# Kernel tuning notes

Hardware: AMD Instinct MI355X
Metric: run time of the kernel (lower is better)

## Reference

```python
import jax, jax.numpy as jnp
import numpy as np

NUM_HEADS = 8
NUM_GROUPS = 32
EPS = 1e-4


def group_norm(x, scale, bias):
    # x: [b, L, C]; normalize over (L, channels-within-group) per flax GroupNorm
    b, l, c = x.shape
    xg = x.reshape(b, l, NUM_GROUPS, c // NUM_GROUPS)
    mean = jnp.mean(xg, axis=(1, 3), keepdims=True)
    var = jnp.var(xg, axis=(1, 3), keepdims=True)
    xg = (xg - mean) * jax.lax.rsqrt(var + EPS)
    return xg.reshape(b, l, c) * scale + bias


def setup_inputs() -> dict:
    key = jax.random.key(0)
    ks = jax.random.split(key, 6)
    bs, L, C = 4, 1024, 512
    hf = C // NUM_HEADS  # 64
    x = jax.random.normal(ks[0], (bs, L, C), dtype=jnp.float32)
    W_qkv = jax.random.normal(ks[1], (C, C * 2), dtype=jnp.float32) * (1.0 / C)
    gn_qkv_scale = jnp.ones((C * 2,), dtype=jnp.float32)
    gn_qkv_bias = jnp.zeros((C * 2,), dtype=jnp.float32)
    rel_emb = jax.random.normal(ks[2], (hf * 2, 2 * L - 1), dtype=jnp.float32) * (1.0 / hf)
    gn_out_scale = jnp.ones((C,), dtype=jnp.float32)
    gn_out_bias = jnp.zeros((C,), dtype=jnp.float32)
    return {
        "x": x,
        "W_qkv": W_qkv,
        "gn_qkv_scale": gn_qkv_scale,
        "gn_qkv_bias": gn_qkv_bias,
        "rel_emb": rel_emb,
        "gn_out_scale": gn_out_scale,
        "gn_out_bias": gn_out_bias,
    }


def reference(x, W_qkv, gn_qkv_scale, gn_qkv_bias, rel_emb, gn_out_scale, gn_out_bias):
    bs, L, C = x.shape
    hf = C // NUM_HEADS
    qkv = x @ W_qkv                                # [b, L, 2C]
    qkv = group_norm(qkv, gn_qkv_scale, gn_qkv_bias)
    qkv = qkv.reshape(bs, L, NUM_HEADS, hf * 2).transpose((0, 2, 3, 1))  # [b,h,2hf,L]
    q = qkv[:, :, : hf // 2]          # [b,h,hf/2,L]
    k = qkv[:, :, hf // 2: hf]        # [b,h,hf/2,L]
    v = qkv[:, :, hf:]                # [b,h,hf,L]
    # relative distance index: rel[i,j] = i - j + L - 1
    rel_idx = jnp.arange(L)[:, None] - jnp.arange(L)[None, :] + (L - 1)
    rpe = rel_emb[:, rel_idx]         # [2hf, L, L]
    rpe_q = rpe[: hf // 2]
    rpe_k = rpe[hf // 2: hf]
    rpe_v = rpe[hf:]
    logits = (
        jnp.einsum('bhdi,bhdj->bhij', q, k)
        + jnp.einsum('bhdi,dij->bhij', q, rpe_k)
        + jnp.einsum('bhdi,dij->bhij', k, rpe_q)
    )
    attn = jax.nn.softmax(logits, axis=3).astype(jnp.float32)
    wv = jnp.einsum('bhij,bhdj->bhdi', attn, v)
    wve = jnp.einsum('bhij,dij->bhdi', attn, rpe_v)
    out = (wv + wve).transpose((0, 3, 1, 2)).reshape(bs, L, C)
    return group_norm(out, gn_out_scale, gn_out_bias)
```

## Files before the change

### kernel.cpp

```cpp
#include <hip/hip_runtime.h>
#include <hip/hip_bf16.h>

typedef unsigned short ushort;
typedef __attribute__((ext_vector_type(8))) short bf16x8;
typedef __attribute__((ext_vector_type(4))) float f32x4;
typedef __attribute__((ext_vector_type(4))) unsigned short ushort4v;

#define BSZ  4
#define LSEQ 1024
#define CIN  512
#define C2   1024
#define NH   8
#define GEPS 1e-4f

static __device__ __forceinline__ ushort f2b(float f) {
    __hip_bfloat16 h = __float2bfloat16(f);
    return *reinterpret_cast<ushort*>(&h);
}
static __device__ __forceinline__ float b2f(ushort u) {
    __hip_bfloat16 h = *reinterpret_cast<__hip_bfloat16*>(&u);
    return __bfloat162float(h);
}

__global__ __launch_bounds__(256) void prep_xsplit(const float* __restrict__ x,
                                                   ushort* __restrict__ xh,
                                                   ushort* __restrict__ xl) {
    const size_t i4 = (size_t)blockIdx.x * 256 + threadIdx.x;
    const float4 v = *reinterpret_cast<const float4*>(&x[i4 * 4]);
    ushort4v h, lo;
    const float vv[4] = {v.x, v.y, v.z, v.w};
    #pragma unroll
    for (int c = 0; c < 4; ++c) {
        const ushort hh = f2b(vv[c]);
        h[c] = hh;
        lo[c] = f2b(vv[c] - b2f(hh));
    }
    *reinterpret_cast<ushort4v*>(&xh[i4 * 4]) = h;
    *reinterpret_cast<ushort4v*>(&xl[i4 * 4]) = lo;
}

__global__ __launch_bounds__(256) void prep_wT(const float* __restrict__ W,
                                               ushort* __restrict__ wth,
                                               ushort* __restrict__ wtl) {
    __shared__ float tl[64][65];
    const int k0 = blockIdx.y * 64, n0 = blockIdx.x * 64;
    const int t = threadIdx.x;
    #pragma unroll
    for (int u = 0; u < 16; ++u) {
        const int idx = t + 256 * u;
        const int kk = idx >> 6, nn = idx & 63;
        tl[kk][nn] = W[(size_t)(k0 + kk) * 1024 + n0 + nn];
    }
    __syncthreads();
    #pragma unroll
    for (int u = 0; u < 16; ++u) {
        const int idx = t + 256 * u;
        const int nn = idx >> 6, kk = idx & 63;
        const float v = tl[kk][nn];
        const ushort h = f2b(v);
        wth[(size_t)(n0 + nn) * 512 + k0 + kk] = h;
        wtl[(size_t)(n0 + nn) * 512 + k0 + kk] = f2b(v - b2f(h));
    }
}

__global__ __launch_bounds__(256) void prep_rel(const float* __restrict__ rel,
                                                ushort* __restrict__ relT,
                                                ushort* __restrict__ relV) {
    const int t = threadIdx.x;
    if (blockIdx.x < 32) {
        __shared__ float tl[64][65];
        const int r0 = blockIdx.x * 64;
        #pragma unroll
        for (int u = 0; u < 16; ++u) {
            const int idx = t + 256 * u;
            const int dd = idx >> 6, rr = idx & 63;
            int r = r0 + rr; if (r > 2046) r = 2046;
            tl[dd][rr] = rel[(size_t)(dd ^ 32) * 2047 + r];
        }
        __syncthreads();
        #pragma unroll
        for (int u = 0; u < 16; ++u) {
            const int idx = t + 256 * u;
            const int rr = idx >> 6, dd = idx & 63;
            relT[(size_t)(r0 + rr) * 64 + dd] = f2b(tl[dd][rr]);
        }
    } else {
        const int idx = (blockIdx.x - 32) * 256 + t;
        const int dv = idx >> 11, r = idx & 2047;
        const int rc = r > 2046 ? 2046 : r;
        relV[(size_t)dv * 2048 + r] = f2b(rel[(size_t)(64 + dv) * 2047 + rc]);
    }
}

__global__ __launch_bounds__(256) void gemm_qkv_mfma(const ushort* __restrict__ xh,
                                                     const ushort* __restrict__ xl,
                                                     const ushort* __restrict__ wth,
                                                     const ushort* __restrict__ wtl,
                                                     float* __restrict__ qkv,
                                                     float* __restrict__ sumq) {
    __shared__ ushort Ah[128][40];
    __shared__ ushort Al[128][40];
    __shared__ ushort Bh[128][40];
    __shared__ ushort Bl[128][40];
    const int t = threadIdx.x;
    const int w = t >> 6, l = t & 63;
    const int lr = l & 15, lq = l >> 4;
    const int wm = w >> 1, wn = w & 1;
    const int m0 = blockIdx.y * 128, n0 = blockIdx.x * 128;
    const int b = m0 >> 10;
    f32x4 acc[4][4] = {};
    for (int k0 = 0; k0 < 512; k0 += 32) {
        __syncthreads();
        #pragma unroll
        for (int u = 0; u < 2; ++u) {
            const int idx = t + 256 * u;
            const int r = idx >> 2, c16 = (idx & 3) * 8;
            *(bf16x8*)&Ah[r][c16] = *(const bf16x8*)&xh[(size_t)(m0 + r) * 512 + k0 + c16];
            *(bf16x8*)&Al[r][c16] = *(const bf16x8*)&xl[(size_t)(m0 + r) * 512 + k0 + c16];
            *(bf16x8*)&Bh[r][c16] = *(const bf16x8*)&wth[(size_t)(n0 + r) * 512 + k0 + c16];
            *(bf16x8*)&Bl[r][c16] = *(const bf16x8*)&wtl[(size_t)(n0 + r) * 512 + k0 + c16];
        }
        __syncthreads();
        bf16x8 ah[4], av[4];
        #pragma unroll
        for (int mi = 0; mi < 4; ++mi) {
            ah[mi] = *(const bf16x8*)&Ah[64 * wm + 16 * mi + lr][8 * lq];
            av[mi] = *(const bf16x8*)&Al[64 * wm + 16 * mi + lr][8 * lq];
        }
        #pragma unroll
        for (int ni = 0; ni < 4; ++ni) {
            const bf16x8 bh = *(const bf16x8*)&Bh[64 * wn + 16 * ni + lr][8 * lq];
            const bf16x8 bl = *(const bf16x8*)&Bl[64 * wn + 16 * ni + lr][8 * lq];
            #pragma unroll
            for (int mi = 0; mi < 4; ++mi) {
                f32x4 a = acc[mi][ni];
                a = __builtin_amdgcn_mfma_f32_16x16x32_bf16(ah[mi], bl, a, 0, 0, 0);
                a = __builtin_amdgcn_mfma_f32_16x16x32_bf16(av[mi], bh, a, 0, 0, 0);
                a = __builtin_amdgcn_mfma_f32_16x16x32_bf16(ah[mi], bh, a, 0, 0, 0);
                acc[mi][ni] = a;
            }
        }
    }
    #pragma unroll
    for (int mi = 0; mi < 4; ++mi)
        #pragma unroll
        for (int ni = 0; ni < 4; ++ni)
            #pragma unroll
            for (int e = 0; e < 4; ++e)
                qkv[(size_t)(m0 + 64 * wm + 16 * mi + 4 * lq + e) * 1024 + n0 + 64 * wn + 16 * ni + lr] = acc[mi][ni][e];
    #pragma unroll
    for (int ni = 0; ni < 4; ++ni) {
        float s = 0.f, s2 = 0.f;
        #pragma unroll
        for (int mi = 0; mi < 4; ++mi)
            #pragma unroll
            for (int e = 0; e < 4; ++e) { const float v = acc[mi][ni][e]; s += v; s2 += v * v; }
        #pragma unroll
        for (int o = 32; o; o >>= 1) { s += __shfl_xor(s, o, 64); s2 += __shfl_xor(s2, o, 64); }
        if (l == 0) {
            const int g = (n0 + 64 * wn + 16 * ni) >> 5;
            atomicAdd(&sumq[(b * 32 + g) * 2 + 0], s);
            atomicAdd(&sumq[(b * 32 + g) * 2 + 1], s2);
        }
    }
}

__global__ __launch_bounds__(256) void gn_apply_bf(const float* __restrict__ qkv,
                                                   const float* __restrict__ sumq,
                                                   const float* __restrict__ scale,
                                                   const float* __restrict__ bias,
                                                   ushort* __restrict__ qg,
                                                   ushort* __restrict__ qlo,
                                                   ushort* __restrict__ vb) {
    __shared__ float tile[64][65];
    const int b  = blockIdx.z;
    const int l0 = blockIdx.y * 64, c0 = blockIdx.x * 64;
    const int t  = threadIdx.x;
    const bool vhalf = (c0 & 64);
    const int h = c0 >> 7;
    #pragma unroll
    for (int u = 0; u < 16; ++u) {
        const int idx = t + 256 * u;
        const int lr = idx >> 6, cr = idx & 63;
        const int c = c0 + cr, g = c >> 5;
        const float s  = sumq[(b * 32 + g) * 2 + 0];
        const float s2 = sumq[(b * 32 + g) * 2 + 1];
        const float mu = s * (1.f / 32768.f);
        const float rr = rsqrtf(fmaxf(s2 * (1.f / 32768.f) - mu * mu, 0.f) + GEPS);
        float v = qkv[(size_t)(b * LSEQ + l0 + lr) * C2 + c];
        v = (v - mu) * rr * scale[c] + bias[c];
        const ushort hi = f2b(v);
        qg[(size_t)(b * LSEQ + l0 + lr) * C2 + c] = hi;
        if (vhalf) tile[lr][cr] = v;
        else qlo[(size_t)(b * LSEQ + l0 + lr) * 512 + h * 64 + cr] = f2b(v - b2f(hi));
    }
    if (vhalf) {
        __syncthreads();
        #pragma unroll
        for (int u = 0; u < 16; ++u) {
            const int idx = t + 256 * u;
            const int cw = idx >> 6, lw = idx & 63;
            vb[((size_t)((b * NH + h) * 64 + cw)) * LSEQ + l0 + lw] = f2b(tile[lw][cw]);
        }
    }
}

__global__ __launch_bounds__(256) void attn_mfma(const ushort* __restrict__ qg,
                                                 const ushort* __restrict__ qlo,
                                                 const ushort* __restrict__ vbuf,
                                                 const ushort* __restrict__ relT,
                                                 const ushort* __restrict__ relV,
                                                 float* __restrict__ aout,
                                                 float* __restrict__ sumo) {
    __shared__ __align__(16) ushort rT[128][72];
    __shared__ __align__(16) ushort rV[64][136];
    __shared__ __align__(16) ushort vj[64][72];
    __shared__ __align__(16) ushort TUb[4][16][88];
    __shared__ __align__(16) ushort Ps[4][16][72];
    __shared__ __align__(16) ushort Pr[4][16][104];

    const int t = threadIdx.x;
    const int w = t >> 6, l = t & 63;
    const int lr = l & 15, lq = l >> 4;
    const int i0 = blockIdx.x * 64;
    const int h = blockIdx.y, b = blockIdx.z;
    const int ck0 = w >> 1;

    const size_t arow = (size_t)(b * LSEQ + i0 + 16 * w + lr);
    const bf16x8 a_q  = *(const bf16x8*)&qg[arow * C2 + h * 128 + 8 * lq];
    const bf16x8 a_k  = *(const bf16x8*)&qg[arow * C2 + h * 128 + 32 + 8 * lq];
    const bf16x8 a_ql = *(const bf16x8*)&qlo[arow * 512 + h * 64 + 8 * lq];

    {
        uint* pz = (uint*)&Pr[w][0][0];
        #pragma unroll
        for (int u = 0; u < 13; ++u) pz[l + 64 * u] = 0;
    }

    float m_r[4], l_r[4];
    #pragma unroll
    for (int e = 0; e < 4; ++e) { m_r[e] = -3.0e38f; l_r[e] = 0.f; }
    f32x4 Oa[4] = {};

    const size_t vbase = (size_t)((b * NH + h) * 64) * LSEQ;
    const int tbase = 4 * lq + 63 - lr;
    const int prbase = 16 * w - 32 * ck0 + 63 + 4 * lq - lr;

    for (int j0 = 0; j0 < LSEQ; j0 += 64) {
        const int r0 = i0 - j0 + 960;
        __syncthreads();
        #pragma unroll
        for (int u = 0; u < 4; ++u) {
            const int idx = t + 256 * u;
            const int rl = idx >> 3, c8 = (idx & 7) * 8;
            *(bf16x8*)&rT[rl][c8] = *(const bf16x8*)&relT[(size_t)(r0 + rl) * 64 + c8];
        }
        #pragma unroll
        for (int u = 0; u < 4; ++u) {
            const int idx = t + 256 * u;
            const int dv = idx >> 4, c8 = (idx & 15) * 8;
            *(bf16x8*)&rV[dv][c8] = *(const bf16x8*)&relV[(size_t)dv * 2048 + r0 + c8];
        }
        #pragma unroll
        for (int u = 0; u < 2; ++u) {
            const int idx = t + 256 * u;
            const int dv = idx >> 3, c8 = (idx & 7) * 8;
            *(bf16x8*)&vj[dv][c8] = *(const bf16x8*)&vbuf[vbase + (size_t)dv * LSEQ + j0 + c8];
        }
        __syncthreads();

        #pragma unroll
        for (int ct5 = 0; ct5 < 5; ++ct5) {
            const int rr = 16 * (w + ct5) + lr;
            f32x4 acc = {0.f, 0.f, 0.f, 0.f};
            acc = __builtin_amdgcn_mfma_f32_16x16x32_bf16(a_q, *(const bf16x8*)&rT[rr][8 * lq], acc, 0, 0, 0);
            acc = __builtin_amdgcn_mfma_f32_16x16x32_bf16(a_k, *(const bf16x8*)&rT[rr][32 + 8 * lq], acc, 0, 0, 0);
            #pragma unroll
            for (int e = 0; e < 4; ++e) TUb[w][4 * lq + e][16 * ct5 + lr] = f2b(acc[e]);
        }

        f32x4 sv[4];
        #pragma unroll
        for (int n = 0; n < 4; ++n) {
            const size_t krow = (size_t)(b * LSEQ + j0 + 16 * n + lr);
            const bf16x8 b_hi = *(const bf16x8*)&qg[krow * C2 + h * 128 + 32 + 8 * lq];
            const bf16x8 b_lo = *(const bf16x8*)&qlo[krow * 512 + h * 64 + 32 + 8 * lq];
            f32x4 acc = {0.f, 0.f, 0.f, 0.f};
            acc = __builtin_amdgcn_mfma_f32_16x16x32_bf16(a_q,  b_lo, acc, 0, 0, 0);
            acc = __builtin_amdgcn_mfma_f32_16x16x32_bf16(a_ql, b_hi, acc, 0, 0, 0);
            acc = __builtin_amdgcn_mfma_f32_16x16x32_bf16(a_q,  b_hi, acc, 0, 0, 0);
            #pragma unroll
            for (int e = 0; e < 4; ++e) acc[e] += b2f(TUb[w][4 * lq + e][tbase + e - 16 * n]);
            sv[n] = acc;
        }

        float mx[4];
        #pragma unroll
        for (int e = 0; e < 4; ++e)
            mx[e] = fmaxf(fmaxf(sv[0][e], sv[1][e]), fmaxf(sv[2][e], sv[3][e]));
        #pragma unroll
        for (int o = 1; o < 16; o <<= 1)
            #pragma unroll
            for (int e = 0; e < 4; ++e) mx[e] = fmaxf(mx[e], __shfl_xor(mx[e], o, 64));
        float alpha[4], ssum[4];
        #pragma unroll
        for (int e = 0; e < 4; ++e) {
            const float mn = fmaxf(m_r[e], mx[e]);
            alpha[e] = __expf(m_r[e] - mn);
            m_r[e] = mn;
            ssum[e] = 0.f;
        }
        #pragma unroll
        for (int n = 0; n < 4; ++n)
            #pragma unroll
            for (int e = 0; e < 4; ++e) {
                const float p = __expf(sv[n][e] - m_r[e]);
                ssum[e] += p;
                const ushort pb = f2b(p);
                Ps[w][4 * lq + e][16 * n + lr] = pb;
                Pr[w][4 * lq + e][prbase + e - 16 * n] = pb;
            }
        #pragma unroll
        for (int o = 1; o < 16; o <<= 1)
            #pragma unroll
            for (int e = 0; e < 4; ++e) ssum[e] += __shfl_xor(ssum[e], o, 64);
        #pragma unroll
        for (int e = 0; e < 4; ++e) l_r[e] = l_r[e] * alpha[e] + ssum[e];

        const bf16x8 pa0 = *(const bf16x8*)&Ps[w][lr][8 * lq];
        const bf16x8 pa1 = *(const bf16x8*)&Ps[w][lr][32 + 8 * lq];
        bf16x8 pra[3];
        #pragma unroll
        for (int kk = 0; kk < 3; ++kk) pra[kk] = *(const bf16x8*)&Pr[w][lr][32 * kk + 8 * lq];
        #pragma unroll
        for (int n = 0; n < 4; ++n) {
            f32x4 acc = Oa[n];
            #pragma unroll
            for (int e = 0; e < 4; ++e) acc[e] *= alpha[e];
            acc = __builtin_amdgcn_mfma_f32_16x16x32_bf16(pa0, *(const bf16x8*)&vj[16 * n + lr][8 * lq], acc, 0, 0, 0);
            acc = __builtin_amdgcn_mfma_f32_16x16x32_bf16(pa1, *(const bf16x8*)&vj[16 * n + lr][32 + 8 * lq], acc, 0, 0, 0);
            #pragma unroll
            for (int kk = 0; kk < 3; ++kk) {
                const bf16x8 brv = *(const bf16x8*)&rV[16 * n + lr][32 * (ck0 + kk) + 8 * lq];
                acc = __builtin_amdgcn_mfma_f32_16x16x32_bf16(pra[kk], brv, acc, 0, 0, 0);
            }
            Oa[n] = acc;
        }
    }

    #pragma unroll
    for (int n = 0; n < 4; ++n) {
        float s = 0.f, s2 = 0.f;
        #pragma unroll
        for (int e = 0; e < 4; ++e) {
            const float o = Oa[n][e] / l_r[e];
            aout[((size_t)(b * LSEQ + i0 + 16 * w + 4 * lq + e)) * CIN + h * 64 + 16 * n + lr] = o;
            s += o; s2 += o * o;
        }
        #pragma unroll
        for (int o = 32; o; o >>= 1) { s += __shfl_xor(s, o, 64); s2 += __shfl_xor(s2, o, 64); }
        if (l == 0) {
            atomicAdd(&sumo[(b * 32 + h * 4 + n) * 2 + 0], s);
            atomicAdd(&sumo[(b * 32 + h * 4 + n) * 2 + 1], s2);
        }
    }
}

__global__ __launch_bounds__(256) void gn_out_apply(const float* __restrict__ aout,
                                                    const float* __restrict__ sumo,
                                                    const float* __restrict__ scale,
                                                    const float* __restrict__ bias,
                                                    float* __restrict__ out) {
    const int idx4 = blockIdx.x * 256 + threadIdx.x;
    const int c = (idx4 & 127) * 4;
    const size_t row = idx4 >> 7;
    const int b = (int)(row >> 10);
    const int g = c >> 4;
    const float s  = sumo[(b * 32 + g) * 2 + 0];
    const float s2 = sumo[(b * 32 + g) * 2 + 1];
    const float mu = s * (1.f / 16384.f);
    const float rr = rsqrtf(fmaxf(s2 * (1.f / 16384.f) - mu * mu, 0.f) + GEPS);
    const float4 v = *reinterpret_cast<const float4*>(&aout[row * 512 + c]);
    const float4 sc = *reinterpret_cast<const float4*>(&scale[c]);
    const float4 bi = *reinterpret_cast<const float4*>(&bias[c]);
    float4 o;
    o.x = (v.x - mu) * rr * sc.x + bi.x;
    o.y = (v.y - mu) * rr * sc.y + bi.y;
    o.z = (v.z - mu) * rr * sc.z + bi.z;
    o.w = (v.w - mu) * rr * sc.w + bi.w;
    *reinterpret_cast<float4*>(&out[row * 512 + c]) = o;
}

extern "C" void kernel_launch(void* const* d_in, const int* in_sizes, int n_in,
                              void* d_out, int out_size, void* d_ws, size_t ws_size,
                              hipStream_t stream) {
    (void)in_sizes; (void)n_in; (void)out_size; (void)ws_size;
    const float* x   = (const float*)d_in[0];
    const float* W   = (const float*)d_in[1];
    const float* gqs = (const float*)d_in[2];
    const float* gqb = (const float*)d_in[3];
    const float* rel = (const float*)d_in[4];
    const float* gos = (const float*)d_in[5];
    const float* gob = (const float*)d_in[6];
    float* out = (float*)d_out;

    char* ws = (char*)d_ws;
    float*  qkv  = (float*)ws;
    ushort* qg   = (ushort*)(ws + (16u << 20));
    ushort* vb   = (ushort*)(ws + (24u << 20));
    ushort* rTb  = (ushort*)(ws + (28u << 20));
    ushort* rVb  = (ushort*)(ws + (28u << 20) + (256u << 10));
    ushort* qlo  = (ushort*)(ws + (28u << 20) + (512u << 10));
    float*  aout = (float*)ws;
    float*  stats = (float*)(ws + (32u << 20) + (512u << 10));
    float* sumq = stats;
    float* sumo = stats + 256;
    ushort* xhi = (ushort*)(ws + (16u << 20));
    ushort* xlo = (ushort*)(ws + (20u << 20));
    ushort* wth = (ushort*)(ws + (24u << 20));
    ushort* wtl = (ushort*)(ws + (25u << 20));

    hipMemsetAsync(stats, 0, 2048, stream);
    prep_xsplit<<<2048, 256, 0, stream>>>(x, xhi, xlo);
    prep_wT<<<dim3(16, 8), 256, 0, stream>>>(W, wth, wtl);
    prep_rel<<<544, 256, 0, stream>>>(rel, rTb, rVb);
    gemm_qkv_mfma<<<dim3(8, 32), 256, 0, stream>>>(xhi, xlo, wth, wtl, qkv, sumq);
    gn_apply_bf<<<dim3(16, 16, BSZ), 256, 0, stream>>>(qkv, sumq, gqs, gqb, qg, qlo, vb);
    attn_mfma<<<dim3(16, NH, BSZ), 256, 0, stream>>>(qg, qlo, vb, rTb, rVb, aout, sumo);
    gn_out_apply<<<2048, 256, 0, stream>>>(aout, sumo, gos, gob, out);
}
```

Measured before the change: 231.9 us.

## Split attention over key halves per block, read operands from global, halve GEMM N tile

The attention kernel now gives each pair of waves one 16-row query tile and splits the key range between them. Each wave runs its own online softmax and the two partial results are merged through shared memory at the end. The shared-memory staging of rel embeddings and V is removed: MFMA operands are loaded straight from global/L2, and per-wave scratch is merged into one buffer to cut LDS use and allow more blocks per CU. The QKV GEMM tile shrinks from 128x128 to 128x64 so the grid doubles. This trades more redundant global loads and an extra merge step for more parallelism and occupancy.

```diff
diff --git a/kernel.cpp b/kernel.cpp
--- a/kernel.cpp
+++ b/kernel.cpp
@@ -100,15 +100,14 @@
                                                      float* __restrict__ sumq) {
     __shared__ ushort Ah[128][40];
     __shared__ ushort Al[128][40];
-    __shared__ ushort Bh[128][40];
-    __shared__ ushort Bl[128][40];
+    __shared__ ushort Bh[64][40];
+    __shared__ ushort Bl[64][40];
     const int t = threadIdx.x;
     const int w = t >> 6, l = t & 63;
     const int lr = l & 15, lq = l >> 4;
-    const int wm = w >> 1, wn = w & 1;
-    const int m0 = blockIdx.y * 128, n0 = blockIdx.x * 128;
+    const int m0 = blockIdx.y * 128, n0 = blockIdx.x * 64;
     const int b = m0 >> 10;
-    f32x4 acc[4][4] = {};
+    f32x4 acc[2][4] = {};
     for (int k0 = 0; k0 < 512; k0 += 32) {
         __syncthreads();
         #pragma unroll
@@ -117,22 +116,25 @@
             const int r = idx >> 2, c16 = (idx & 3) * 8;
             *(bf16x8*)&Ah[r][c16] = *(const bf16x8*)&xh[(size_t)(m0 + r) * 512 + k0 + c16];
             *(bf16x8*)&Al[r][c16] = *(const bf16x8*)&xl[(size_t)(m0 + r) * 512 + k0 + c16];
+        }
+        {
+            const int r = t >> 2, c16 = (t & 3) * 8;
             *(bf16x8*)&Bh[r][c16] = *(const bf16x8*)&wth[(size_t)(n0 + r) * 512 + k0 + c16];
             *(bf16x8*)&Bl[r][c16] = *(const bf16x8*)&wtl[(size_t)(n0 + r) * 512 + k0 + c16];
         }
         __syncthreads();
-        bf16x8 ah[4], av[4];
-        #pragma unroll
-        for (int mi = 0; mi < 4; ++mi) {
-            ah[mi] = *(const bf16x8*)&Ah[64 * wm + 16 * mi + lr][8 * lq];
-            av[mi] = *(const bf16x8*)&Al[64 * wm + 16 * mi + lr][8 * lq];
+        bf16x8 ah[2], av[2];
+        #pragma unroll
+        for (int mi = 0; mi < 2; ++mi) {
+            ah[mi] = *(const bf16x8*)&Ah[32 * w + 16 * mi + lr][8 * lq];
+            av[mi] = *(const bf16x8*)&Al[32 * w + 16 * mi + lr][8 * lq];
         }
         #pragma unroll
         for (int ni = 0; ni < 4; ++ni) {
-            const bf16x8 bh = *(const bf16x8*)&Bh[64 * wn + 16 * ni + lr][8 * lq];
-            const bf16x8 bl = *(const bf16x8*)&Bl[64 * wn + 16 * ni + lr][8 * lq];
-            #pragma unroll
-            for (int mi = 0; mi < 4; ++mi) {
+            const bf16x8 bh = *(const bf16x8*)&Bh[16 * ni + lr][8 * lq];
+            const bf16x8 bl = *(const bf16x8*)&Bl[16 * ni + lr][8 * lq];
+            #pragma unroll
+            for (int mi = 0; mi < 2; ++mi) {
                 f32x4 a = acc[mi][ni];
                 a = __builtin_amdgcn_mfma_f32_16x16x32_bf16(ah[mi], bl, a, 0, 0, 0);
                 a = __builtin_amdgcn_mfma_f32_16x16x32_bf16(av[mi], bh, a, 0, 0, 0);
@@ -142,23 +144,23 @@
         }
     }
     #pragma unroll
-    for (int mi = 0; mi < 4; ++mi)
+    for (int mi = 0; mi < 2; ++mi)
         #pragma unroll
         for (int ni = 0; ni < 4; ++ni)
             #pragma unroll
             for (int e = 0; e < 4; ++e)
-                qkv[(size_t)(m0 + 64 * wm + 16 * mi + 4 * lq + e) * 1024 + n0 + 64 * wn + 16 * ni + lr] = acc[mi][ni][e];
+                qkv[(size_t)(m0 + 32 * w + 16 * mi + 4 * lq + e) * 1024 + n0 + 16 * ni + lr] = acc[mi][ni][e];
     #pragma unroll
     for (int ni = 0; ni < 4; ++ni) {
         float s = 0.f, s2 = 0.f;
         #pragma unroll
-        for (int mi = 0; mi < 4; ++mi)
+        for (int mi = 0; mi < 2; ++mi)
             #pragma unroll
             for (int e = 0; e < 4; ++e) { const float v = acc[mi][ni][e]; s += v; s2 += v * v; }
         #pragma unroll
         for (int o = 32; o; o >>= 1) { s += __shfl_xor(s, o, 64); s2 += __shfl_xor(s2, o, 64); }
         if (l == 0) {
-            const int g = (n0 + 64 * wn + 16 * ni) >> 5;
+            const int g = (n0 + 16 * ni) >> 5;
             atomicAdd(&sumq[(b * 32 + g) * 2 + 0], s);
             atomicAdd(&sumq[(b * 32 + g) * 2 + 1], s2);
         }
@@ -205,78 +207,52 @@
     }
 }
 
-__global__ __launch_bounds__(256) void attn_mfma(const ushort* __restrict__ qg,
-                                                 const ushort* __restrict__ qlo,
-                                                 const ushort* __restrict__ vbuf,
-                                                 const ushort* __restrict__ relT,
-                                                 const ushort* __restrict__ relV,
-                                                 float* __restrict__ aout,
-                                                 float* __restrict__ sumo) {
-    __shared__ __align__(16) ushort rT[128][72];
-    __shared__ __align__(16) ushort rV[64][136];
-    __shared__ __align__(16) ushort vj[64][72];
-    __shared__ __align__(16) ushort TUb[4][16][88];
-    __shared__ __align__(16) ushort Ps[4][16][72];
-    __shared__ __align__(16) ushort Pr[4][16][104];
+__global__ __launch_bounds__(256, 4) void attn_mfma(const ushort* __restrict__ qg,
+                                                    const ushort* __restrict__ qlo,
+                                                    const ushort* __restrict__ vbuf,
+                                                    const ushort* __restrict__ relT,
+                                                    const ushort* __restrict__ relV,
+                                                    float* __restrict__ aout,
+                                                    float* __restrict__ sumo) {
+    __shared__ __align__(16) ushort wscr[4][16][264];
 
     const int t = threadIdx.x;
     const int w = t >> 6, l = t & 63;
     const int lr = l & 15, lq = l >> 4;
-    const int i0 = blockIdx.x * 64;
     const int h = blockIdx.y, b = blockIdx.z;
-    const int ck0 = w >> 1;
-
-    const size_t arow = (size_t)(b * LSEQ + i0 + 16 * w + lr);
+    const int i0s = blockIdx.x * 32 + (w >> 1) * 16;
+    const int jh = w & 1;
+
+    for (int idx = l; idx < 16 * 52; idx += 64) {
+        const int row = idx / 52, c = idx % 52;
+        *(unsigned int*)&wscr[w][row][160 + 2 * c] = 0;
+    }
+
+    const size_t arow = (size_t)(b * LSEQ + i0s + lr);
     const bf16x8 a_q  = *(const bf16x8*)&qg[arow * C2 + h * 128 + 8 * lq];
     const bf16x8 a_k  = *(const bf16x8*)&qg[arow * C2 + h * 128 + 32 + 8 * lq];
     const bf16x8 a_ql = *(const bf16x8*)&qlo[arow * 512 + h * 64 + 8 * lq];
 
-    {
-        uint* pz = (uint*)&Pr[w][0][0];
-        #pragma unroll
-        for (int u = 0; u < 13; ++u) pz[l + 64 * u] = 0;
-    }
-
     float m_r[4], l_r[4];
     #pragma unroll
     for (int e = 0; e < 4; ++e) { m_r[e] = -3.0e38f; l_r[e] = 0.f; }
     f32x4 Oa[4] = {};
 
-    const size_t vbase = (size_t)((b * NH + h) * 64) * LSEQ;
-    const int tbase = 4 * lq + 63 - lr;
-    const int prbase = 16 * w - 32 * ck0 + 63 + 4 * lq - lr;
-
-    for (int j0 = 0; j0 < LSEQ; j0 += 64) {
-        const int r0 = i0 - j0 + 960;
-        __syncthreads();
-        #pragma unroll
-        for (int u = 0; u < 4; ++u) {
-            const int idx = t + 256 * u;
-            const int rl = idx >> 3, c8 = (idx & 7) * 8;
-            *(bf16x8*)&rT[rl][c8] = *(const bf16x8*)&relT[(size_t)(r0 + rl) * 64 + c8];
-        }
-        #pragma unroll
-        for (int u = 0; u < 4; ++u) {
-            const int idx = t + 256 * u;
-            const int dv = idx >> 4, c8 = (idx & 15) * 8;
-            *(bf16x8*)&rV[dv][c8] = *(const bf16x8*)&relV[(size_t)dv * 2048 + r0 + c8];
-        }
-        #pragma unroll
-        for (int u = 0; u < 2; ++u) {
-            const int idx = t + 256 * u;
-            const int dv = idx >> 3, c8 = (idx & 7) * 8;
-            *(bf16x8*)&vj[dv][c8] = *(const bf16x8*)&vbuf[vbase + (size_t)dv * LSEQ + j0 + c8];
-        }
-        __syncthreads();
-
-        #pragma unroll
-        for (int ct5 = 0; ct5 < 5; ++ct5) {
-            const int rr = 16 * (w + ct5) + lr;
+    const int tb = 4 * lq + 63 - lr;
+    const size_t vrow0 = (size_t)((b * NH + h) * 64);
+
+    for (int it = 0; it < 8; ++it) {
+        const int j0 = jh * 512 + it * 64;
+        const int r0 = i0s - j0 + 960;
+
+        #pragma unroll
+        for (int ct = 0; ct < 5; ++ct) {
+            const size_t rr = (size_t)(r0 + 16 * ct + lr) * 64;
             f32x4 acc = {0.f, 0.f, 0.f, 0.f};
-            acc = __builtin_amdgcn_mfma_f32_16x16x32_bf16(a_q, *(const bf16x8*)&rT[rr][8 * lq], acc, 0, 0, 0);
-            acc = __builtin_amdgcn_mfma_f32_16x16x32_bf16(a_k, *(const bf16x8*)&rT[rr][32 + 8 * lq], acc, 0, 0, 0);
-            #pragma unroll
-            for (int e = 0; e < 4; ++e) TUb[w][4 * lq + e][16 * ct5 + lr] = f2b(acc[e]);
+            acc = __builtin_amdgcn_mfma_f32_16x16x32_bf16(a_q, *(const bf16x8*)&relT[rr + 8 * lq], acc, 0, 0, 0);
+            acc = __builtin_amdgcn_mfma_f32_16x16x32_bf16(a_k, *(const bf16x8*)&relT[rr + 32 + 8 * lq], acc, 0, 0, 0);
+            #pragma unroll
+            for (int e = 0; e < 4; ++e) wscr[w][4 * lq + e][16 * ct + lr] = f2b(acc[e]);
         }
 
         f32x4 sv[4];
@@ -290,7 +266,7 @@
             acc = __builtin_amdgcn_mfma_f32_16x16x32_bf16(a_ql, b_hi, acc, 0, 0, 0);
             acc = __builtin_amdgcn_mfma_f32_16x16x32_bf16(a_q,  b_hi, acc, 0, 0, 0);
             #pragma unroll
-            for (int e = 0; e < 4; ++e) acc[e] += b2f(TUb[w][4 * lq + e][tbase + e - 16 * n]);
+            for (int e = 0; e < 4; ++e) acc[e] += b2f(wscr[w][4 * lq + e][tb + e - 16 * n]);
             sv[n] = acc;
         }
 
@@ -317,8 +293,8 @@
                 const float p = __expf(sv[n][e] - m_r[e]);
                 ssum[e] += p;
                 const ushort pb = f2b(p);
-                Ps[w][4 * lq + e][16 * n + lr] = pb;
-                Pr[w][4 * lq + e][prbase + e - 16 * n] = pb;
+                wscr[w][4 * lq + e][88 + 16 * n + lr] = pb;
+                wscr[w][4 * lq + e][160 + tb + e - 16 * n] = pb;
             }
         #pragma unroll
         for (int o = 1; o < 16; o <<= 1)
@@ -327,41 +303,62 @@
         #pragma unroll
         for (int e = 0; e < 4; ++e) l_r[e] = l_r[e] * alpha[e] + ssum[e];
 
-        const bf16x8 pa0 = *(const bf16x8*)&Ps[w][lr][8 * lq];
-        const bf16x8 pa1 = *(const bf16x8*)&Ps[w][lr][32 + 8 * lq];
+        const bf16x8 pa0 = *(const bf16x8*)&wscr[w][lr][88 + 8 * lq];
+        const bf16x8 pa1 = *(const bf16x8*)&wscr[w][lr][88 + 32 + 8 * lq];
         bf16x8 pra[3];
         #pragma unroll
-        for (int kk = 0; kk < 3; ++kk) pra[kk] = *(const bf16x8*)&Pr[w][lr][32 * kk + 8 * lq];
+        for (int kk = 0; kk < 3; ++kk) pra[kk] = *(const bf16x8*)&wscr[w][lr][160 + 32 * kk + 8 * lq];
         #pragma unroll
         for (int n = 0; n < 4; ++n) {
+            const size_t vr = (vrow0 + 16 * n + lr) * LSEQ;
+            const size_t rvr = (size_t)(16 * n + lr) * 2048 + r0;
             f32x4 acc = Oa[n];
             #pragma unroll
             for (int e = 0; e < 4; ++e) acc[e] *= alpha[e];
-            acc = __builtin_amdgcn_mfma_f32_16x16x32_bf16(pa0, *(const bf16x8*)&vj[16 * n + lr][8 * lq], acc, 0, 0, 0);
-            acc = __builtin_amdgcn_mfma_f32_16x16x32_bf16(pa1, *(const bf16x8*)&vj[16 * n + lr][32 + 8 * lq], acc, 0, 0, 0);
+            acc = __builtin_amdgcn_mfma_f32_16x16x32_bf16(pa0, *(const bf16x8*)&vbuf[vr + j0 + 8 * lq], acc, 0, 0, 0);
+            acc = __builtin_amdgcn_mfma_f32_16x16x32_bf16(pa1, *(const bf16x8*)&vbuf[vr + j0 + 32 + 8 * lq], acc, 0, 0, 0);
             #pragma unroll
             for (int kk = 0; kk < 3; ++kk) {
-                const bf16x8 brv = *(const bf16x8*)&rV[16 * n + lr][32 * (ck0 + kk) + 8 * lq];
-                acc = __builtin_amdgcn_mfma_f32_16x16x32_bf16(pra[kk], brv, acc, 0, 0, 0);
+                acc = __builtin_amdgcn_mfma_f32_16x16x32_bf16(pra[kk], *(const bf16x8*)&relV[rvr + 32 * kk + 8 * lq], acc, 0, 0, 0);
             }
             Oa[n] = acc;
         }
     }
 
-    #pragma unroll
-    for (int n = 0; n < 4; ++n) {
-        float s = 0.f, s2 = 0.f;
+    float* fs = (float*)&wscr[w][0][0];
+    #pragma unroll
+    for (int n = 0; n < 4; ++n)
+        #pragma unroll
+        for (int e = 0; e < 4; ++e) fs[(4 * n + e) * 64 + l] = Oa[n][e];
+    #pragma unroll
+    for (int e = 0; e < 4; ++e) { fs[(16 + e) * 64 + l] = m_r[e]; fs[(20 + e) * 64 + l] = l_r[e]; }
+    __syncthreads();
+    if (jh == 0) {
+        const float* fp = (const float*)&wscr[w + 1][0][0];
+        float a0[4], a1[4], Li[4];
         #pragma unroll
         for (int e = 0; e < 4; ++e) {
-            const float o = Oa[n][e] / l_r[e];
-            aout[((size_t)(b * LSEQ + i0 + 16 * w + 4 * lq + e)) * CIN + h * 64 + 16 * n + lr] = o;
-            s += o; s2 += o * o;
-        }
-        #pragma unroll
-        for (int o = 32; o; o >>= 1) { s += __shfl_xor(s, o, 64); s2 += __shfl_xor(s2, o, 64); }
-        if (l == 0) {
-            atomicAdd(&sumo[(b * 32 + h * 4 + n) * 2 + 0], s);
-            atomicAdd(&sumo[(b * 32 + h * 4 + n) * 2 + 1], s2);
+            const float m1 = fp[(16 + e) * 64 + l], l1 = fp[(20 + e) * 64 + l];
+            const float mn = fmaxf(m_r[e], m1);
+            a0[e] = __expf(m_r[e] - mn);
+            a1[e] = __expf(m1 - mn);
+            Li[e] = 1.f / (l_r[e] * a0[e] + l1 * a1[e]);
+        }
+        #pragma unroll
+        for (int n = 0; n < 4; ++n) {
+            float s = 0.f, s2 = 0.f;
+            #pragma unroll
+            for (int e = 0; e < 4; ++e) {
+                const float o = (Oa[n][e] * a0[e] + fp[(4 * n + e) * 64 + l] * a1[e]) * Li[e];
+                aout[(size_t)(b * LSEQ + i0s + 4 * lq + e) * CIN + h * 64 + 16 * n + lr] = o;
+                s += o; s2 += o * o;
+            }
+            #pragma unroll
+            for (int o = 32; o; o >>= 1) { s += __shfl_xor(s, o, 64); s2 += __shfl_xor(s2, o, 64); }
+            if (l == 0) {
+                atomicAdd(&sumo[(b * 32 + h * 4 + n) * 2 + 0], s);
+                atomicAdd(&sumo[(b * 32 + h * 4 + n) * 2 + 1], s2);
+            }
         }
     }
 }
@@ -424,8 +421,8 @@
     prep_xsplit<<<2048, 256, 0, stream>>>(x, xhi, xlo);
     prep_wT<<<dim3(16, 8), 256, 0, stream>>>(W, wth, wtl);
     prep_rel<<<544, 256, 0, stream>>>(rel, rTb, rVb);
-    gemm_qkv_mfma<<<dim3(8, 32), 256, 0, stream>>>(xhi, xlo, wth, wtl, qkv, sumq);
+    gemm_qkv_mfma<<<dim3(16, 32), 256, 0, stream>>>(xhi, xlo, wth, wtl, qkv, sumq);
     gn_apply_bf<<<dim3(16, 16, BSZ), 256, 0, stream>>>(qkv, sumq, gqs, gqb, qg, qlo, vb);
-    attn_mfma<<<dim3(16, NH, BSZ), 256, 0, stream>>>(qg, qlo, vb, rTb, rVb, aout, sumo);
+    attn_mfma<<<dim3(32, NH, BSZ), 256, 0, stream>>>(qg, qlo, vb, rTb, rVb, aout, sumo);
     gn_out_apply<<<2048, 256, 0, stream>>>(aout, sumo, gos, gob, out);
 }
```

Measured after the change: 316.2 us. +36.4%, slower.
